# Kernel optimization log

Hardware: AMD Instinct MI355X
Metric: run time of the kernel (lower is better)

The kernel has to match this reference:

```python
import jax, jax.numpy as jnp
import numpy as np

BS, N, D_IN, D_OUT = 4, 512, 64, 64
TEMP = 1.0
POOL_K = 0.5
N_KEEP = max(int(N * POOL_K), 1)  # 256
BN_EPS = 1e-5


def setup_inputs() -> dict:
    key = jax.random.key(0)
    ks = jax.random.split(key, 12)
    xav = lambda k, shape: jax.random.normal(k, shape, jnp.float32) * np.sqrt(2.0 / sum(shape))
    return {
        "x": jax.random.normal(ks[0], (BS, N, D_IN), jnp.float32),
        "att_proj_w": xav(ks[1], (D_IN, D_OUT)),
        "att_proj_b": jnp.zeros((D_OUT,), jnp.float32),
        "att_weight": xav(ks[2], (D_OUT, 1))[:, 0],  # (D_OUT,)
        "pwa_w": xav(ks[3], (D_IN, D_OUT)),
        "pwa_b": jnp.zeros((D_OUT,), jnp.float32),
        "pwoa_w": xav(ks[4], (D_IN, D_OUT)),
        "pwoa_b": jnp.zeros((D_OUT,), jnp.float32),
        "bn_gamma": jnp.ones((D_OUT,), jnp.float32),
        "bn_beta": jnp.zeros((D_OUT,), jnp.float32),
        "bn_mean": jnp.zeros((D_OUT,), jnp.float32),
        "bn_var": jnp.ones((D_OUT,), jnp.float32),
        "pool_w": xav(ks[5], (D_OUT, 1))[:, 0],  # (D_OUT,)
        "pool_b": jnp.zeros((), jnp.float32),
    }


def reference(x, att_proj_w, att_proj_b, att_weight, pwa_w, pwa_b,
              pwoa_w, pwoa_b, bn_gamma, bn_beta, bn_mean, bn_var,
              pool_w, pool_b):
    # ---- GraphAttentionLayer (eval mode: dropout off, BN uses running stats) ----
    # pairwise node product: (bs, i, j, d)
    pair = x[:, :, None, :] * x[:, None, :, :]
    a = jnp.tanh(jnp.einsum('bijd,de->bije', pair, att_proj_w) + att_proj_b)
    scores = jnp.einsum('bije,e->bij', a, att_weight) / TEMP
    att = jax.nn.softmax(scores, axis=-1)  # torch softmax over dim=-2 of (bs,i,j,1) == j axis
    agg = jnp.einsum('bij,bjd->bid', att, x)
    h = (agg @ pwa_w + pwa_b) + (x @ pwoa_w + pwoa_b)
    h = (h - bn_mean) * jax.lax.rsqrt(bn_var + BN_EPS) * bn_gamma + bn_beta
    h = jax.nn.selu(h)
    # ---- GraphPool (eval: dropout off) ----
    s = jax.nn.sigmoid(h @ pool_w + pool_b)  # (bs, N)
    _, idx = jax.lax.top_k(s, N_KEEP)        # (bs, N_KEEP), sorted desc like torch.topk
    hs = h * s[..., None]
    out = jnp.take_along_axis(hs, idx[..., None], axis=1)  # (bs, N_KEEP, D_OUT)
    return out
```

## Files before the change

kernel.cpp:

```cpp
#include <hip/hip_runtime.h>
#include <hip/hip_bf16.h>
#include <math.h>

#define BSZ 4
#define NN 512
#define DD 64
#define NKEEP 256

typedef __attribute__((ext_vector_type(8))) short short8;
typedef __attribute__((ext_vector_type(4))) float f32x4;

__device__ __forceinline__ ushort f2bf_rne(float f) {
  union { float f; unsigned u; } v; v.f = f;
  unsigned r = v.u + 0x7fffu + ((v.u >> 16) & 1u);
  return (ushort)(r >> 16);
}
__device__ __forceinline__ float bf2f(ushort h) {
  union { unsigned u; float f; } v; v.u = ((unsigned)h) << 16;
  return v.f;
}
__device__ __forceinline__ void split2(float a, float b, uint& hu, uint& lu) {
  const ushort ha = f2bf_rne(a), hb = f2bf_rne(b);
  hu = (uint)ha | ((uint)hb << 16);
  const ushort la = f2bf_rne(a - bf2f(ha));
  const ushort lb = f2bf_rne(b - bf2f(hb));
  lu = (uint)la | ((uint)lb << 16);
}

__global__ void k_prep(const float* __restrict__ apw,
                       ushort* __restrict__ wht, ushort* __restrict__ wlt,
                       int* __restrict__ tile_tab) {
  const int idx = blockIdx.x * 256 + threadIdx.x;
  const int d = idx >> 6, e = idx & 63;
  const float wv = apw[idx];
  const ushort h = f2bf_rne(wv);
  const ushort lo = f2bf_rne(wv - bf2f(h));
  wht[e * 64 + d] = h;
  wlt[e * 64 + d] = lo;
  if (idx < 528) {
    int it = 0;
    #pragma unroll
    for (int r = 1; r < 32; ++r) it += ((r * (65 - r)) / 2 <= idx);
    const int jt = it + (idx - (it * (65 - it)) / 2);
    tile_tab[idx] = it | (jt << 8);
  }
}

__global__ __launch_bounds__(64) void k_score(
    const float* __restrict__ x, const ushort* __restrict__ wht,
    const ushort* __restrict__ wlt, const float* __restrict__ apb,
    const float* __restrict__ aw, const int* __restrict__ tile_tab,
    float* __restrict__ sT) {
  __shared__ __align__(16) float T[16][16];

  const int l = threadIdx.x;
  const int il = l & 15, g = l >> 4;
  const int gid = blockIdx.x;
  const int b = gid / 528;
  const int pid = gid - b * 528;
  const int pk = tile_tab[pid];
  const int it = pk & 0xff, jt = pk >> 8;
  const int i0 = it * 16, j0 = jt * 16;
  const bool diag = (it == jt);

  const float* xb = x + (size_t)b * NN * DD;
  float* plane = sT + (size_t)b * NN * NN;

  short8 wfh[4][2], wfl[4][2];
  #pragma unroll
  for (int eq = 0; eq < 4; ++eq)
    #pragma unroll
    for (int ks = 0; ks < 2; ++ks) {
      const int off = (eq * 16 + il) * 64 + ks * 32 + g * 8;
      wfh[eq][ks] = *reinterpret_cast<const short8*>(wht + off);
      wfl[eq][ks] = *reinterpret_cast<const short8*>(wlt + off);
    }

  const float K2 = 2.8853900817779268f;
  float aw2_4[4], bK2[4], awq = 0.f;
  #pragma unroll
  for (int eq = 0; eq < 4; ++eq) {
    const float a = aw[eq * 16 + il];
    aw2_4[eq] = 2.f * a;
    bK2[eq] = apb[eq * 16 + il] * K2;
    awq += a;
  }
  awq += __shfl_xor(awq, 1, 64);
  awq += __shfl_xor(awq, 2, 64);
  awq += __shfl_xor(awq, 4, 64);
  awq += __shfl_xor(awq, 8, 64);
  const float awC = awq;

  const float* xjr = xb + (size_t)(j0 + il) * DD;
  const float4 xj0 = *reinterpret_cast<const float4*>(xjr + g * 8);
  const float4 xj1 = *reinterpret_cast<const float4*>(xjr + g * 8 + 4);
  const float4 xj2 = *reinterpret_cast<const float4*>(xjr + 32 + g * 8);
  const float4 xj3 = *reinterpret_cast<const float4*>(xjr + 32 + g * 8 + 4);

  #pragma unroll 2
  for (int ii = 0; ii < 16; ++ii) {
    const int i_glob = i0 + ii;
    const float* xir = xb + (size_t)i_glob * DD;
    const float4 xi0 = *reinterpret_cast<const float4*>(xir + g * 8);
    const float4 xi1 = *reinterpret_cast<const float4*>(xir + g * 8 + 4);
    const float4 xi2 = *reinterpret_cast<const float4*>(xir + 32 + g * 8);
    const float4 xi3 = *reinterpret_cast<const float4*>(xir + 32 + g * 8 + 4);

    union { uint u[4]; short8 s; } hA, lA, hB, lB;
    split2(xj0.x * xi0.x, xj0.y * xi0.y, hA.u[0], lA.u[0]);
    split2(xj0.z * xi0.z, xj0.w * xi0.w, hA.u[1], lA.u[1]);
    split2(xj1.x * xi1.x, xj1.y * xi1.y, hA.u[2], lA.u[2]);
    split2(xj1.z * xi1.z, xj1.w * xi1.w, hA.u[3], lA.u[3]);
    split2(xj2.x * xi2.x, xj2.y * xi2.y, hB.u[0], lB.u[0]);
    split2(xj2.z * xi2.z, xj2.w * xi2.w, hB.u[1], lB.u[1]);
    split2(xj3.x * xi3.x, xj3.y * xi3.y, hB.u[2], lB.u[2]);
    split2(xj3.z * xi3.z, xj3.w * xi3.w, hB.u[3], lB.u[3]);

    f32x4 acc[4];
    #pragma unroll
    for (int eq = 0; eq < 4; ++eq) acc[eq] = (f32x4){0.f, 0.f, 0.f, 0.f};
    #pragma unroll
    for (int eq = 0; eq < 4; ++eq) {
      acc[eq] = __builtin_amdgcn_mfma_f32_16x16x32_bf16(hA.s, wfh[eq][0], acc[eq], 0, 0, 0);
      acc[eq] = __builtin_amdgcn_mfma_f32_16x16x32_bf16(hA.s, wfl[eq][0], acc[eq], 0, 0, 0);
      acc[eq] = __builtin_amdgcn_mfma_f32_16x16x32_bf16(lA.s, wfh[eq][0], acc[eq], 0, 0, 0);
      acc[eq] = __builtin_amdgcn_mfma_f32_16x16x32_bf16(hB.s, wfh[eq][1], acc[eq], 0, 0, 0);
      acc[eq] = __builtin_amdgcn_mfma_f32_16x16x32_bf16(hB.s, wfl[eq][1], acc[eq], 0, 0, 0);
      acc[eq] = __builtin_amdgcn_mfma_f32_16x16x32_bf16(lB.s, wfh[eq][1], acc[eq], 0, 0, 0);
    }

    float neg[4] = {0.f, 0.f, 0.f, 0.f};
    #pragma unroll
    for (int eq = 0; eq < 4; ++eq)
      #pragma unroll
      for (int rr = 0; rr < 4; ++rr) {
        const float ex = __builtin_amdgcn_exp2f(fmaf(acc[eq][rr], K2, bK2[eq]));
        const float rc = __builtin_amdgcn_rcpf(ex + 1.0f);
        neg[rr] = fmaf(aw2_4[eq], rc, neg[rr]);
      }
    #pragma unroll
    for (int rr = 0; rr < 4; ++rr) {
      neg[rr] += __shfl_xor(neg[rr], 1, 64);
      neg[rr] += __shfl_xor(neg[rr], 2, 64);
      neg[rr] += __shfl_xor(neg[rr], 4, 64);
      neg[rr] += __shfl_xor(neg[rr], 8, 64);
    }
    const f32x4 sc = {awC - neg[0], awC - neg[1], awC - neg[2], awC - neg[3]};

    if (il == 0) {
      if (!diag) {
        *reinterpret_cast<f32x4*>(plane + (size_t)i_glob * NN + j0 + g * 4) = sc;
      } else {
        #pragma unroll
        for (int rr = 0; rr < 4; ++rr) {
          const int jv = j0 + g * 4 + rr;
          if (jv >= i_glob) plane[(size_t)i_glob * NN + jv] = sc[rr];
        }
      }
      *reinterpret_cast<f32x4*>(&T[ii][g * 4]) = sc;
    }
  }

  __syncthreads();

  {
    const int jv = il;
    const float m0 = T[g * 4 + 0][jv];
    const float m1 = T[g * 4 + 1][jv];
    const float m2 = T[g * 4 + 2][jv];
    const float m3 = T[g * 4 + 3][jv];
    if (!diag) {
      const f32x4 mv = {m0, m1, m2, m3};
      *reinterpret_cast<f32x4*>(plane + (size_t)(j0 + jv) * NN + i0 + g * 4) = mv;
    } else {
      const int jr = j0 + jv;
      if (jr > i0 + g * 4 + 0) plane[(size_t)jr * NN + i0 + g * 4 + 0] = m0;
      if (jr > i0 + g * 4 + 1) plane[(size_t)jr * NN + i0 + g * 4 + 1] = m1;
      if (jr > i0 + g * 4 + 2) plane[(size_t)jr * NN + i0 + g * 4 + 2] = m2;
      if (jr > i0 + g * 4 + 3) plane[(size_t)jr * NN + i0 + g * 4 + 3] = m3;
    }
  }
}

__global__ __launch_bounds__(256) void k_soft(
    const float* __restrict__ x, const float* __restrict__ sT,
    const float* __restrict__ pwa, const float* __restrict__ pwab,
    const float* __restrict__ pwoa, const float* __restrict__ pwob,
    const float* __restrict__ gam, const float* __restrict__ bet,
    const float* __restrict__ mu, const float* __restrict__ var,
    const float* __restrict__ poolw, const float* __restrict__ poolb,
    float* __restrict__ h, float* __restrict__ s) {
  __shared__ float ssc[2][512];
  __shared__ float srm[2][4], srs[2][4];
  __shared__ float sagg[4][2][64];
  __shared__ float rag[2][64], xis[2][64];

  const int t = threadIdx.x;
  const int w = t >> 6, l = t & 63;
  const int b = blockIdx.x >> 8;
  const int rp = blockIdx.x & 255;
  const int i_r0 = rp * 2, i_r1 = i_r0 + 1;
  const float* xb = x + (size_t)b * NN * DD;
  const float* pl0 = sT + (size_t)b * NN * NN;
  const int jw = w * 128;

  const size_t o0 = (size_t)i_r0 * NN + jw + l;
  const size_t o1 = (size_t)i_r1 * NN + jw + l;
  float r0a = pl0[o0];
  float r0b = pl0[o0 + 64];
  float r1a = pl0[o1];
  float r1b = pl0[o1 + 64];
  float m0 = fmaxf(r0a, r0b), m1 = fmaxf(r1a, r1b);
  #pragma unroll
  for (int off = 32; off; off >>= 1) {
    m0 = fmaxf(m0, __shfl_xor(m0, off, 64));
    m1 = fmaxf(m1, __shfl_xor(m1, off, 64));
  }
  if (l == 0) { srm[0][w] = m0; srm[1][w] = m1; }
  __syncthreads();
  m0 = fmaxf(fmaxf(srm[0][0], srm[0][1]), fmaxf(srm[0][2], srm[0][3]));
  m1 = fmaxf(fmaxf(srm[1][0], srm[1][1]), fmaxf(srm[1][2], srm[1][3]));

  const float L2E = 1.4426950408889634f;
  float e0a = __builtin_amdgcn_exp2f((r0a - m0) * L2E);
  float e0b = __builtin_amdgcn_exp2f((r0b - m0) * L2E);
  float e1a = __builtin_amdgcn_exp2f((r1a - m1) * L2E);
  float e1b = __builtin_amdgcn_exp2f((r1b - m1) * L2E);
  float ps0 = e0a + e0b, ps1 = e1a + e1b;
  #pragma unroll
  for (int off = 32; off; off >>= 1) {
    ps0 += __shfl_xor(ps0, off, 64);
    ps1 += __shfl_xor(ps1, off, 64);
  }
  if (l == 0) { srs[0][w] = ps0; srs[1][w] = ps1; }
  __syncthreads();
  const float inv0 = 1.f / (srs[0][0] + srs[0][1] + srs[0][2] + srs[0][3]);
  const float inv1 = 1.f / (srs[1][0] + srs[1][1] + srs[1][2] + srs[1][3]);
  ssc[0][jw + l] = e0a * inv0;
  ssc[0][jw + 64 + l] = e0b * inv0;
  ssc[1][jw + l] = e1a * inv1;
  ssc[1][jw + 64 + l] = e1b * inv1;
  __syncthreads();

  float g0a = 0.f, g0b = 0.f, g1a = 0.f, g1b = 0.f;
  #pragma unroll 4
  for (int jj = 0; jj < 128; jj += 2) {
    const int j = jw + jj;
    const float xv0 = xb[(size_t)j * DD + l];
    const float xv1 = xb[(size_t)(j + 1) * DD + l];
    g0a = fmaf(ssc[0][j], xv0, g0a);
    g1a = fmaf(ssc[1][j], xv0, g1a);
    g0b = fmaf(ssc[0][j + 1], xv1, g0b);
    g1b = fmaf(ssc[1][j + 1], xv1, g1b);
  }
  sagg[w][0][l] = g0a + g0b;
  sagg[w][1][l] = g1a + g1b;
  __syncthreads();

  if (w < 2) {
    const int irow = i_r0 + w;
    rag[w][l] = sagg[0][w][l] + sagg[1][w][l] + sagg[2][w][l] + sagg[3][w][l];
    xis[w][l] = xb[(size_t)irow * DD + l];
    float acc = 0.f;
    #pragma unroll 8
    for (int d = 0; d < 64; ++d) {
      acc = fmaf(rag[w][d], pwa[d * 64 + l], acc);
      acc = fmaf(xis[w][d], pwoa[d * 64 + l], acc);
    }
    acc += pwab[l] + pwob[l];
    float hb = (acc - mu[l]) * rsqrtf(var[l] + 1e-5f) * gam[l] + bet[l];
    const float SC = 1.0507009873554805f, AL = 1.6732632423543772f;
    float hv = hb > 0.f ? SC * hb : SC * AL * expm1f(hb);
    h[((size_t)(b * NN + irow)) * DD + l] = hv;

    float p = hv * poolw[l];
    #pragma unroll
    for (int off = 32; off; off >>= 1) p += __shfl_xor(p, off, 64);
    if (l == 0) s[b * NN + irow] = 1.f / (1.f + expf(-(p + poolb[0])));
  }
}

__global__ __launch_bounds__(512) void k_sel(
    const float* __restrict__ s, const float* __restrict__ h,
    float* __restrict__ out) {
  __shared__ float svv[NN];
  __shared__ int inv[NKEEP];
  __shared__ float sval[NKEEP];
  const int b = blockIdx.x, t = threadIdx.x;
  svv[t] = s[b * NN + t];
  __syncthreads();

  const float my = svv[t];
  int r = 0;
  #pragma unroll 4
  for (int j0 = 0; j0 < NN; j0 += 4) {
    float4 v = *reinterpret_cast<const float4*>(&svv[j0]);
    r += (v.x > my) || (v.x == my && (j0 + 0) < t);
    r += (v.y > my) || (v.y == my && (j0 + 1) < t);
    r += (v.z > my) || (v.z == my && (j0 + 2) < t);
    r += (v.w > my) || (v.w == my && (j0 + 3) < t);
  }
  if (r < NKEEP) { inv[r] = t; sval[r] = my; }
  __syncthreads();

  #pragma unroll
  for (int pos = t; pos < NKEEP * 16; pos += 512) {
    const int kk = pos >> 4, d4 = (pos & 15) * 4;
    const int i = inv[kk];
    const float sc = sval[kk];
    float4 v = *reinterpret_cast<const float4*>(
        h + ((size_t)(b * NN + i)) * DD + d4);
    v.x *= sc; v.y *= sc; v.z *= sc; v.w *= sc;
    *reinterpret_cast<float4*>(out + ((size_t)(b * NKEEP + kk)) * DD + d4) = v;
  }
}

extern "C" void kernel_launch(void* const* d_in, const int* in_sizes, int n_in,
                              void* d_out, int out_size, void* d_ws, size_t ws_size,
                              hipStream_t stream) {
  const float* x     = (const float*)d_in[0];
  const float* apw   = (const float*)d_in[1];
  const float* apb   = (const float*)d_in[2];
  const float* aw    = (const float*)d_in[3];
  const float* pwa   = (const float*)d_in[4];
  const float* pwab  = (const float*)d_in[5];
  const float* pwoa  = (const float*)d_in[6];
  const float* pwob  = (const float*)d_in[7];
  const float* gam   = (const float*)d_in[8];
  const float* bet   = (const float*)d_in[9];
  const float* mu    = (const float*)d_in[10];
  const float* var   = (const float*)d_in[11];
  const float* poolw = (const float*)d_in[12];
  const float* poolb = (const float*)d_in[13];
  float* out = (float*)d_out;

  float* sT    = (float*)d_ws;
  float* h     = sT + (size_t)BSZ * NN * NN;
  float* s     = h + (size_t)BSZ * NN * DD;
  ushort* wht  = (ushort*)(s + BSZ * NN);
  ushort* wlt  = wht + 4096;
  int* tile_tab = (int*)(wlt + 4096);

  k_prep<<<16, 256, 0, stream>>>(apw, wht, wlt, tile_tab);
  k_score<<<2112, 64, 0, stream>>>(x, wht, wlt, apb, aw, tile_tab, sT);
  k_soft<<<BSZ * 256, 256, 0, stream>>>(x, sT, pwa, pwab, pwoa, pwob,
                                        gam, bet, mu, var, poolw, poolb, h, s);
  k_sel<<<BSZ, 512, 0, stream>>>(s, h, out);
}
```

Baseline: 76.65 us.

## Halve score tile height to 8 rows and use truncation bf16 split

The symmetric score kernel now works on 8x16 tiles instead of 16x16. That doubles the block count to 4224 so more wavefronts run across the CUs, and the tile table and the transpose write-back are rebuilt to match. The hi/lo bf16 split of the pairwise products now uses plain truncation by bit masking instead of round-to-nearest-even, which removes ALU work per element. Truncation keeps the hi+lo representation nearly exact, but the residual is truncated too, so precision drops slightly. Smaller tiles also mean less reuse of the per-block weight fragment loads.

```diff
diff --git a/kernel.cpp b/kernel.cpp
--- a/kernel.cpp
+++ b/kernel.cpp
@@ -19,12 +19,12 @@
   union { unsigned u; float f; } v; v.u = ((unsigned)h) << 16;
   return v.f;
 }
-__device__ __forceinline__ void split2(float a, float b, uint& hu, uint& lu) {
-  const ushort ha = f2bf_rne(a), hb = f2bf_rne(b);
-  hu = (uint)ha | ((uint)hb << 16);
-  const ushort la = f2bf_rne(a - bf2f(ha));
-  const ushort lb = f2bf_rne(b - bf2f(hb));
-  lu = (uint)la | ((uint)lb << 16);
+__device__ __forceinline__ void split2t(float a, float b, uint& hu, uint& lu) {
+  const uint au = __float_as_uint(a), bu = __float_as_uint(b);
+  hu = (au >> 16) | (bu & 0xffff0000u);
+  const float ra = a - __uint_as_float(au & 0xffff0000u);
+  const float rb = b - __uint_as_float(bu & 0xffff0000u);
+  lu = (__float_as_uint(ra) >> 16) | (__float_as_uint(rb) & 0xffff0000u);
 }
 
 __global__ void k_prep(const float* __restrict__ apw,
@@ -37,11 +37,10 @@
   const ushort lo = f2bf_rne(wv - bf2f(h));
   wht[e * 64 + d] = h;
   wlt[e * 64 + d] = lo;
-  if (idx < 528) {
-    int it = 0;
-    #pragma unroll
-    for (int r = 1; r < 32; ++r) it += ((r * (65 - r)) / 2 <= idx);
-    const int jt = it + (idx - (it * (65 - it)) / 2);
+  if (idx < 1056) {
+    int it = 0, rem = idx;
+    while (rem >= 32 - (it >> 1)) { rem -= 32 - (it >> 1); ++it; }
+    const int jt = (it >> 1) + rem;
     tile_tab[idx] = it | (jt << 8);
   }
 }
@@ -51,17 +50,17 @@
     const ushort* __restrict__ wlt, const float* __restrict__ apb,
     const float* __restrict__ aw, const int* __restrict__ tile_tab,
     float* __restrict__ sT) {
-  __shared__ __align__(16) float T[16][16];
+  __shared__ __align__(16) float T[8][16];
 
   const int l = threadIdx.x;
   const int il = l & 15, g = l >> 4;
   const int gid = blockIdx.x;
-  const int b = gid / 528;
-  const int pid = gid - b * 528;
+  const int b = gid / 1056;
+  const int pid = gid - b * 1056;
   const int pk = tile_tab[pid];
   const int it = pk & 0xff, jt = pk >> 8;
-  const int i0 = it * 16, j0 = jt * 16;
-  const bool diag = (it == jt);
+  const int i0 = it * 8, j0 = jt * 16;
+  const bool diag = ((it >> 1) == jt);
 
   const float* xb = x + (size_t)b * NN * DD;
   float* plane = sT + (size_t)b * NN * NN;
@@ -98,7 +97,7 @@
   const float4 xj3 = *reinterpret_cast<const float4*>(xjr + 32 + g * 8 + 4);
 
   #pragma unroll 2
-  for (int ii = 0; ii < 16; ++ii) {
+  for (int ii = 0; ii < 8; ++ii) {
     const int i_glob = i0 + ii;
     const float* xir = xb + (size_t)i_glob * DD;
     const float4 xi0 = *reinterpret_cast<const float4*>(xir + g * 8);
@@ -107,14 +106,14 @@
     const float4 xi3 = *reinterpret_cast<const float4*>(xir + 32 + g * 8 + 4);
 
     union { uint u[4]; short8 s; } hA, lA, hB, lB;
-    split2(xj0.x * xi0.x, xj0.y * xi0.y, hA.u[0], lA.u[0]);
-    split2(xj0.z * xi0.z, xj0.w * xi0.w, hA.u[1], lA.u[1]);
-    split2(xj1.x * xi1.x, xj1.y * xi1.y, hA.u[2], lA.u[2]);
-    split2(xj1.z * xi1.z, xj1.w * xi1.w, hA.u[3], lA.u[3]);
-    split2(xj2.x * xi2.x, xj2.y * xi2.y, hB.u[0], lB.u[0]);
-    split2(xj2.z * xi2.z, xj2.w * xi2.w, hB.u[1], lB.u[1]);
-    split2(xj3.x * xi3.x, xj3.y * xi3.y, hB.u[2], lB.u[2]);
-    split2(xj3.z * xi3.z, xj3.w * xi3.w, hB.u[3], lB.u[3]);
+    split2t(xj0.x * xi0.x, xj0.y * xi0.y, hA.u[0], lA.u[0]);
+    split2t(xj0.z * xi0.z, xj0.w * xi0.w, hA.u[1], lA.u[1]);
+    split2t(xj1.x * xi1.x, xj1.y * xi1.y, hA.u[2], lA.u[2]);
+    split2t(xj1.z * xi1.z, xj1.w * xi1.w, hA.u[3], lA.u[3]);
+    split2t(xj2.x * xi2.x, xj2.y * xi2.y, hB.u[0], lB.u[0]);
+    split2t(xj2.z * xi2.z, xj2.w * xi2.w, hB.u[1], lB.u[1]);
+    split2t(xj3.x * xi3.x, xj3.y * xi3.y, hB.u[2], lB.u[2]);
+    split2t(xj3.z * xi3.z, xj3.w * xi3.w, hB.u[3], lB.u[3]);
 
     f32x4 acc[4];
     #pragma unroll
@@ -164,20 +163,17 @@
   __syncthreads();
 
   {
-    const int jv = il;
-    const float m0 = T[g * 4 + 0][jv];
-    const float m1 = T[g * 4 + 1][jv];
-    const float m2 = T[g * 4 + 2][jv];
-    const float m3 = T[g * 4 + 3][jv];
+    const int jv = l >> 2;
+    const int ip = (l & 3) * 2;
+    const float m0 = T[ip + 0][jv];
+    const float m1 = T[ip + 1][jv];
+    const int jr = j0 + jv;
     if (!diag) {
-      const f32x4 mv = {m0, m1, m2, m3};
-      *reinterpret_cast<f32x4*>(plane + (size_t)(j0 + jv) * NN + i0 + g * 4) = mv;
+      const float2 mv = {m0, m1};
+      *reinterpret_cast<float2*>(plane + (size_t)jr * NN + i0 + ip) = mv;
     } else {
-      const int jr = j0 + jv;
-      if (jr > i0 + g * 4 + 0) plane[(size_t)jr * NN + i0 + g * 4 + 0] = m0;
-      if (jr > i0 + g * 4 + 1) plane[(size_t)jr * NN + i0 + g * 4 + 1] = m1;
-      if (jr > i0 + g * 4 + 2) plane[(size_t)jr * NN + i0 + g * 4 + 2] = m2;
-      if (jr > i0 + g * 4 + 3) plane[(size_t)jr * NN + i0 + g * 4 + 3] = m3;
+      if (jr > i0 + ip + 0) plane[(size_t)jr * NN + i0 + ip + 0] = m0;
+      if (jr > i0 + ip + 1) plane[(size_t)jr * NN + i0 + ip + 1] = m1;
     }
   }
 }
@@ -342,7 +338,7 @@
   int* tile_tab = (int*)(wlt + 4096);
 
   k_prep<<<16, 256, 0, stream>>>(apw, wht, wlt, tile_tab);
-  k_score<<<2112, 64, 0, stream>>>(x, wht, wlt, apb, aw, tile_tab, sT);
+  k_score<<<4224, 64, 0, stream>>>(x, wht, wlt, apb, aw, tile_tab, sT);
   k_soft<<<BSZ * 256, 256, 0, stream>>>(x, sT, pwa, pwab, pwoa, pwob,
                                         gam, bet, mu, var, poolw, poolb, h, s);
   k_sel<<<BSZ, 512, 0, stream>>>(s, h, out);
```

Measured after the change: 70.12 us. -8.5%, faster.
